# Kernel optimization log

Measured on AMD Instinct MI355X. Metric: run time of the kernel, lower is better.

The kernel has to match this reference:

```python
import jax, jax.numpy as jnp
import numpy as np

D_MODEL = 1024
NHEAD = 16
HEAD_DIM = D_MODEL // NHEAD


def setup_inputs() -> dict:
    key = jax.random.key(0)
    ks = jax.random.split(key, 11)
    B, T = 2, 2048
    s = 1.0 / np.sqrt(D_MODEL)
    return {
        "query": jax.random.normal(ks[0], (B, T, D_MODEL), jnp.float32),
        "key": jax.random.normal(ks[1], (B, T, D_MODEL), jnp.float32),
        "value": jax.random.normal(ks[2], (B, T, D_MODEL), jnp.float32),
        "Wq": jax.random.normal(ks[3], (D_MODEL, D_MODEL), jnp.float32) * s,
        "bq": jnp.zeros((D_MODEL,), jnp.float32),
        "Wk": jax.random.normal(ks[4], (D_MODEL, D_MODEL), jnp.float32) * s,
        "bk": jnp.zeros((D_MODEL,), jnp.float32),
        "Wv": jax.random.normal(ks[5], (D_MODEL, D_MODEL), jnp.float32) * s,
        "bv": jnp.zeros((D_MODEL,), jnp.float32),
        "Wo": jax.random.normal(ks[6], (D_MODEL, D_MODEL), jnp.float32) * s,
        "bo": jnp.zeros((D_MODEL,), jnp.float32),
    }


def reference(query, key, value, Wq, bq, Wk, bk, Wv, bv, Wo, bo):
    B, T, _ = query.shape
    scale = HEAD_DIM ** -0.5
    # Linear projections (torch Linear: x @ W.T + b)
    Q = query @ Wq.T + bq
    K = key @ Wk.T + bk
    V = value @ Wv.T + bv
    # [B, H, T, hd]
    Q = Q.reshape(B, T, NHEAD, HEAD_DIM).transpose(0, 2, 1, 3)
    K = K.reshape(B, T, NHEAD, HEAD_DIM).transpose(0, 2, 1, 3)
    V = V.reshape(B, T, NHEAD, HEAD_DIM).transpose(0, 2, 1, 3)
    # Attention scores [B, H, T, T]
    scores = jnp.einsum("bhqd,bhkd->bhqk", Q, K) * scale
    probs = jax.nn.softmax(scores, axis=-1)
    # dropout is identity in eval mode
    out = jnp.einsum("bhqk,bhkd->bhqd", probs, V)
    out = out.transpose(0, 2, 1, 3).reshape(B, T, D_MODEL)
    return out @ Wo.T + bo
```

## Files before the change

kernel.cpp:

```cpp
#include <hip/hip_runtime.h>
#include <stdint.h>

#define LOG2E_OVER_SQRTHD 0.18033688011112042f
#define SM_BIAS 12.0f

typedef unsigned short u16;
typedef _Float16 f16;
typedef __attribute__((ext_vector_type(4))) float f32x4;
typedef __attribute__((ext_vector_type(8))) _Float16 f16x8;

static __device__ __forceinline__ u16 f2h_bits(float f) {
  union { f16 h; u16 u; } v; v.h = (f16)f; return v.u;
}

static __device__ __forceinline__ void g2l16(const void* g, void* l) {
  __builtin_amdgcn_global_load_lds((const __attribute__((address_space(1))) void*)g,
                                   (__attribute__((address_space(3))) void*)l,
                                   16, 0, 0);
}

__global__ __launch_bounds__(256) void pack_all(
    const float* __restrict__ q, const float* __restrict__ k, const float* __restrict__ v,
    const float* __restrict__ wq, const float* __restrict__ wk,
    const float* __restrict__ wv, const float* __restrict__ wo,
    u16* __restrict__ X, u16* __restrict__ W) {
  int flat = blockIdx.x * 256 + threadIdx.x;
  const float* src;
  u16* dst;
  int idx;
  if (flat < 3 * 1048576) {
    int z = flat >> 20;
    idx = flat & 1048575;
    src = (z == 0) ? q : (z == 1) ? k : v;
    dst = X + (size_t)z * 4194304;
  } else {
    int f2 = flat - 3 * 1048576;
    int z = f2 >> 18;
    idx = f2 & 262143;
    src = (z == 0) ? wq : (z == 1) ? wk : (z == 2) ? wv : wo;
    dst = W + (size_t)z * 1048576;
  }
  float4 x = ((const float4*)src)[idx];
  ushort4 o;
  o.x = f2h_bits(x.x); o.y = f2h_bits(x.y); o.z = f2h_bits(x.z); o.w = f2h_bits(x.w);
  *(ushort4*)(dst + (size_t)idx * 4) = o;
}

template <bool OUT_F16>
static __device__ __forceinline__ void gemm_body(
    const u16* __restrict__ A, const u16* __restrict__ W,
    const float* __restrict__ bias, void* __restrict__ C,
    int ldc, bool row_bias, float oscale, int bm, int bn) {
  __shared__ u16 As[128 * 32];
  __shared__ u16 Bs[128 * 32];
  const int tid = threadIdx.x;
  const int lane = tid & 63;
  const int wave = tid >> 6;
  const int wm = wave >> 1, wn = wave & 1;
  const int quad = lane >> 4, l15 = lane & 15;

  f32x4 acc[4][4] = {};

  const int r0 = tid >> 2;
  const int c0 = (tid & 3) * 8;
  const u16* Ab = A + (size_t)bm * 1024;
  const u16* Wb = W + (size_t)bn * 1024;

  for (int kt = 0; kt < 32; ++kt) {
    const int kc = kt * 32;
    g2l16(Ab + (size_t)r0 * 1024 + kc + c0, As + tid * 8);
    g2l16(Ab + (size_t)(r0 + 64) * 1024 + kc + c0, As + (256 + tid) * 8);
    g2l16(Wb + (size_t)r0 * 1024 + kc + c0, Bs + tid * 8);
    g2l16(Wb + (size_t)(r0 + 64) * 1024 + kc + c0, Bs + (256 + tid) * 8);
    __syncthreads();
    f16x8 af[4], bw[4];
#pragma unroll
    for (int mt = 0; mt < 4; ++mt)
      af[mt] = *(const f16x8*)(As + (wm * 64 + mt * 16 + l15) * 32 + quad * 8);
#pragma unroll
    for (int nt = 0; nt < 4; ++nt)
      bw[nt] = *(const f16x8*)(Bs + (wn * 64 + nt * 16 + l15) * 32 + quad * 8);
#pragma unroll
    for (int mt = 0; mt < 4; ++mt)
#pragma unroll
      for (int nt = 0; nt < 4; ++nt)
        acc[mt][nt] = __builtin_amdgcn_mfma_f32_16x16x32_f16(af[mt], bw[nt], acc[mt][nt], 0, 0, 0);
    __syncthreads();
  }

#pragma unroll
  for (int mt = 0; mt < 4; ++mt) {
    const int row = bm + wm * 64 + mt * 16 + quad * 4;
#pragma unroll
    for (int nt = 0; nt < 4; ++nt) {
      const int col = bn + wn * 64 + nt * 16 + l15;
      const float bcol = row_bias ? 0.0f : bias[col];
#pragma unroll
      for (int i = 0; i < 4; ++i) {
        const float bb = row_bias ? bias[row + i] : bcol;
        float val = (acc[mt][nt][i] + bb) * oscale;
        if (OUT_F16)
          ((u16*)C)[(size_t)(row + i) * ldc + col] = f2h_bits(val);
        else
          ((float*)C)[(size_t)(row + i) * ldc + col] = val;
      }
    }
  }
}

__global__ __launch_bounds__(256) void gemm_qkv(const u16* __restrict__ X,
    const u16* __restrict__ Wf, const float* __restrict__ bq,
    const float* __restrict__ bk, const float* __restrict__ bv,
    u16* __restrict__ QK, u16* __restrict__ Vt, float qscale) {
  const int z = blockIdx.z;
  if (z == 0) {
    gemm_body<true>(X, Wf, bq, QK, 1024, false, qscale,
                    blockIdx.x * 128, blockIdx.y * 128);
  } else if (z == 1) {
    gemm_body<true>(X + (size_t)4194304, Wf + (size_t)1048576, bk,
                    QK + (size_t)4194304, 1024, false, 1.0f,
                    blockIdx.x * 128, blockIdx.y * 128);
  } else {
    gemm_body<true>(Wf + (size_t)2 * 1048576, X + (size_t)2 * 4194304, bv,
                    Vt, 4096, true, 1.0f,
                    blockIdx.y * 128, blockIdx.x * 128);
  }
}

__global__ __launch_bounds__(256) void gemm_out(const u16* __restrict__ O,
    const u16* __restrict__ Wo, const float* __restrict__ bo,
    float* __restrict__ out) {
  gemm_body<false>(O, Wo, bo, out, 1024, false, 1.0f,
                   blockIdx.x * 128, blockIdx.y * 128);
}

__global__ __launch_bounds__(256) void attn_kernel(const u16* __restrict__ QK,
                                                   const u16* __restrict__ Vt,
                                                   u16* __restrict__ O) {
  constexpr int LSP = 68;
  __shared__ u16 Qs[64 * 64];
  __shared__ u16 Ks[64 * 64];
  __shared__ u16 Vts[64 * 64];
  __shared__ u16 Ps[4][16 * LSP];

  const u16* Qb = QK;
  const u16* Kb = QK + (size_t)4096 * 1024;

  const int tid = threadIdx.x, lane = tid & 63, wave = tid >> 6;
  const int quad = lane >> 4, l15 = lane & 15;
  const int qt = blockIdx.x, h = blockIdx.y, b = blockIdx.z;
  const size_t qrow0 = (size_t)b * 2048 + qt * 64;
  const size_t kv0 = (size_t)b * 2048;
  const int hc = h * 64;

  const int r0 = tid >> 3;
  const int p0 = tid & 7;
  const int s0 = (p0 ^ (r0 & 7)) * 8;

  g2l16(Qb + (qrow0 + r0) * 1024 + hc + s0, Qs + tid * 8);
  g2l16(Qb + (qrow0 + 32 + r0) * 1024 + hc + s0, Qs + (256 + tid) * 8);
  __syncthreads();

  const int Rq = wave * 16 + l15;
  const f16x8 aq0 = *(const f16x8*)(Qs + Rq * 64 + ((quad ^ (Rq & 7)) * 8));
  const f16x8 aq1 = *(const f16x8*)(Qs + Rq * 64 + (((quad + 4) ^ (Rq & 7)) * 8));

  f32x4 o_acc[4] = {};
  float l_part[4] = {0.f, 0.f, 0.f, 0.f};
  u16* Pw = Ps[wave];

  for (int kt = 0; kt < 32; ++kt) {
    const size_t kr0 = kv0 + (size_t)kt * 64;
    __syncthreads();
    g2l16(Kb + (kr0 + r0) * 1024 + hc + s0, Ks + tid * 8);
    g2l16(Kb + (kr0 + 32 + r0) * 1024 + hc + s0, Ks + (256 + tid) * 8);
    g2l16(Vt + (size_t)(hc + r0) * 4096 + kr0 + s0, Vts + tid * 8);
    g2l16(Vt + (size_t)(hc + 32 + r0) * 4096 + kr0 + s0, Vts + (256 + tid) * 8);
    __syncthreads();

    f32x4 s[4];
#pragma unroll
    for (int nt = 0; nt < 4; ++nt)
      s[nt] = f32x4{-SM_BIAS, -SM_BIAS, -SM_BIAS, -SM_BIAS};
#pragma unroll
    for (int nt = 0; nt < 4; ++nt) {
      const int Rk = nt * 16 + l15;
      f16x8 bk0 = *(const f16x8*)(Ks + Rk * 64 + ((quad ^ (Rk & 7)) * 8));
      f16x8 bk1 = *(const f16x8*)(Ks + Rk * 64 + (((quad + 4) ^ (Rk & 7)) * 8));
      s[nt] = __builtin_amdgcn_mfma_f32_16x16x32_f16(aq0, bk0, s[nt], 0, 0, 0);
      s[nt] = __builtin_amdgcn_mfma_f32_16x16x32_f16(aq1, bk1, s[nt], 0, 0, 0);
    }

#pragma unroll
    for (int nt = 0; nt < 4; ++nt)
#pragma unroll
      for (int i = 0; i < 4; ++i) {
        float p = __builtin_amdgcn_exp2f(s[nt][i]);
        l_part[i] += p;
        Pw[(quad * 4 + i) * LSP + nt * 16 + l15] = f2h_bits(p);
      }
    asm volatile("s_waitcnt lgkmcnt(0)" ::: "memory");

    union { f16x8 v; struct { uint2 lo, hi; } h; } ap0, ap1;
    ap0.h.lo = *(const uint2*)(Pw + l15 * LSP + quad * 8);
    ap0.h.hi = *(const uint2*)(Pw + l15 * LSP + quad * 8 + 4);
    ap1.h.lo = *(const uint2*)(Pw + l15 * LSP + 32 + quad * 8);
    ap1.h.hi = *(const uint2*)(Pw + l15 * LSP + 32 + quad * 8 + 4);
#pragma unroll
    for (int ct = 0; ct < 4; ++ct) {
      const int Rv = ct * 16 + l15;
      f16x8 bv0 = *(const f16x8*)(Vts + Rv * 64 + ((quad ^ (Rv & 7)) * 8));
      f16x8 bv1 = *(const f16x8*)(Vts + Rv * 64 + (((quad + 4) ^ (Rv & 7)) * 8));
      o_acc[ct] = __builtin_amdgcn_mfma_f32_16x16x32_f16(ap0.v, bv0, o_acc[ct], 0, 0, 0);
      o_acc[ct] = __builtin_amdgcn_mfma_f32_16x16x32_f16(ap1.v, bv1, o_acc[ct], 0, 0, 0);
    }
  }

#pragma unroll
  for (int i = 0; i < 4; ++i)
#pragma unroll
    for (int d = 1; d < 16; d <<= 1) l_part[i] += __shfl_xor(l_part[i], d);

#pragma unroll
  for (int i = 0; i < 4; ++i) {
    const float inv = 1.0f / l_part[i];
    const size_t row = qrow0 + wave * 16 + quad * 4 + i;
#pragma unroll
    for (int ct = 0; ct < 4; ++ct) {
      float ov = o_acc[ct][i] * inv;
      int col = hc + ct * 16 + l15;
      O[row * 1024 + col] = f2h_bits(ov);
    }
  }
}

extern "C" void kernel_launch(void* const* d_in, const int* in_sizes, int n_in,
                              void* d_out, int out_size, void* d_ws, size_t ws_size,
                              hipStream_t stream) {
  const float* query = (const float*)d_in[0];
  const float* key   = (const float*)d_in[1];
  const float* value = (const float*)d_in[2];
  const float* Wq = (const float*)d_in[3];
  const float* bq = (const float*)d_in[4];
  const float* Wk = (const float*)d_in[5];
  const float* bk = (const float*)d_in[6];
  const float* Wv = (const float*)d_in[7];
  const float* bv = (const float*)d_in[8];
  const float* Wo = (const float*)d_in[9];
  const float* bo = (const float*)d_in[10];
  float* out = (float*)d_out;

  u16* X  = (u16*)d_ws;
  u16* W  = X + (size_t)3 * 4194304;
  u16* QK = W + (size_t)4 * 1048576;
  u16* Vt = QK + (size_t)2 * 4194304;
  u16* O  = X;

  pack_all<<<dim3(16384, 1, 1), 256, 0, stream>>>(query, key, value, Wq, Wk, Wv, Wo, X, W);
  gemm_qkv<<<dim3(32, 8, 3), 256, 0, stream>>>(X, W, bq, bk, bv, QK, Vt,
                                               LOG2E_OVER_SQRTHD);
  attn_kernel<<<dim3(32, 16, 2), 256, 0, stream>>>(QK, Vt, O);
  gemm_out<<<dim3(32, 8, 1), 256, 0, stream>>>(O, W + (size_t)3 * 1048576, bo, out);
}
```

Baseline: 253.3 us.

## Double-buffer LDS tiles in the projection GEMMs and the attention loop

The GEMM body and the attention kernel now keep two LDS buffers for the streamed operands (A/W tiles, and K/Vt tiles). The next K-step's global-to-LDS loads are issued before computing on the current buffer, with one barrier per iteration instead of two. The aim is to overlap global memory latency with MFMA work. In exchange, LDS use roughly doubles for these tiles, which may lower occupancy, especially in the attention kernel.

```diff
diff --git a/kernel.cpp b/kernel.cpp
--- a/kernel.cpp
+++ b/kernel.cpp
@@ -51,8 +51,8 @@
     const u16* __restrict__ A, const u16* __restrict__ W,
     const float* __restrict__ bias, void* __restrict__ C,
     int ldc, bool row_bias, float oscale, int bm, int bn) {
-  __shared__ u16 As[128 * 32];
-  __shared__ u16 Bs[128 * 32];
+  __shared__ u16 As[2][128 * 32];
+  __shared__ u16 Bs[2][128 * 32];
   const int tid = threadIdx.x;
   const int lane = tid & 63;
   const int wave = tid >> 6;
@@ -63,23 +63,31 @@
 
   const int r0 = tid >> 2;
   const int c0 = (tid & 3) * 8;
-  const u16* Ab = A + (size_t)bm * 1024;
-  const u16* Wb = W + (size_t)bn * 1024;
+  const u16* Ab = A + (size_t)bm * 1024 + (size_t)r0 * 1024 + c0;
+  const u16* Wb = W + (size_t)bn * 1024 + (size_t)r0 * 1024 + c0;
+
+  g2l16(Ab, As[0] + tid * 8);
+  g2l16(Ab + 64 * 1024, As[0] + (256 + tid) * 8);
+  g2l16(Wb, Bs[0] + tid * 8);
+  g2l16(Wb + 64 * 1024, Bs[0] + (256 + tid) * 8);
+  __syncthreads();
 
   for (int kt = 0; kt < 32; ++kt) {
-    const int kc = kt * 32;
-    g2l16(Ab + (size_t)r0 * 1024 + kc + c0, As + tid * 8);
-    g2l16(Ab + (size_t)(r0 + 64) * 1024 + kc + c0, As + (256 + tid) * 8);
-    g2l16(Wb + (size_t)r0 * 1024 + kc + c0, Bs + tid * 8);
-    g2l16(Wb + (size_t)(r0 + 64) * 1024 + kc + c0, Bs + (256 + tid) * 8);
-    __syncthreads();
+    const int p = kt & 1;
+    if (kt + 1 < 32) {
+      const int kc = (kt + 1) * 32;
+      g2l16(Ab + kc, As[p ^ 1] + tid * 8);
+      g2l16(Ab + 64 * 1024 + kc, As[p ^ 1] + (256 + tid) * 8);
+      g2l16(Wb + kc, Bs[p ^ 1] + tid * 8);
+      g2l16(Wb + 64 * 1024 + kc, Bs[p ^ 1] + (256 + tid) * 8);
+    }
     f16x8 af[4], bw[4];
 #pragma unroll
     for (int mt = 0; mt < 4; ++mt)
-      af[mt] = *(const f16x8*)(As + (wm * 64 + mt * 16 + l15) * 32 + quad * 8);
+      af[mt] = *(const f16x8*)(As[p] + (wm * 64 + mt * 16 + l15) * 32 + quad * 8);
 #pragma unroll
     for (int nt = 0; nt < 4; ++nt)
-      bw[nt] = *(const f16x8*)(Bs + (wn * 64 + nt * 16 + l15) * 32 + quad * 8);
+      bw[nt] = *(const f16x8*)(Bs[p] + (wn * 64 + nt * 16 + l15) * 32 + quad * 8);
 #pragma unroll
     for (int mt = 0; mt < 4; ++mt)
 #pragma unroll
@@ -139,8 +147,8 @@
                                                    u16* __restrict__ O) {
   constexpr int LSP = 68;
   __shared__ u16 Qs[64 * 64];
-  __shared__ u16 Ks[64 * 64];
-  __shared__ u16 Vts[64 * 64];
+  __shared__ u16 Ks[2][64 * 64];
+  __shared__ u16 Vts[2][64 * 64];
   __shared__ u16 Ps[4][16 * LSP];
 
   const u16* Qb = QK;
@@ -157,8 +165,15 @@
   const int p0 = tid & 7;
   const int s0 = (p0 ^ (r0 & 7)) * 8;
 
+  const u16* Kbase = Kb + (kv0 + r0) * 1024 + hc + s0;
+  const u16* Vbase = Vt + (size_t)(hc + r0) * 4096 + kv0 + s0;
+
   g2l16(Qb + (qrow0 + r0) * 1024 + hc + s0, Qs + tid * 8);
   g2l16(Qb + (qrow0 + 32 + r0) * 1024 + hc + s0, Qs + (256 + tid) * 8);
+  g2l16(Kbase, Ks[0] + tid * 8);
+  g2l16(Kbase + 32 * 1024, Ks[0] + (256 + tid) * 8);
+  g2l16(Vbase, Vts[0] + tid * 8);
+  g2l16(Vbase + (size_t)32 * 4096, Vts[0] + (256 + tid) * 8);
   __syncthreads();
 
   const int Rq = wave * 16 + l15;
@@ -170,13 +185,15 @@
   u16* Pw = Ps[wave];
 
   for (int kt = 0; kt < 32; ++kt) {
-    const size_t kr0 = kv0 + (size_t)kt * 64;
-    __syncthreads();
-    g2l16(Kb + (kr0 + r0) * 1024 + hc + s0, Ks + tid * 8);
-    g2l16(Kb + (kr0 + 32 + r0) * 1024 + hc + s0, Ks + (256 + tid) * 8);
-    g2l16(Vt + (size_t)(hc + r0) * 4096 + kr0 + s0, Vts + tid * 8);
-    g2l16(Vt + (size_t)(hc + 32 + r0) * 4096 + kr0 + s0, Vts + (256 + tid) * 8);
-    __syncthreads();
+    const int p = kt & 1;
+    if (kt + 1 < 32) {
+      const u16* Kn = Kbase + (size_t)(kt + 1) * 64 * 1024;
+      const u16* Vn = Vbase + (size_t)(kt + 1) * 64;
+      g2l16(Kn, Ks[p ^ 1] + tid * 8);
+      g2l16(Kn + 32 * 1024, Ks[p ^ 1] + (256 + tid) * 8);
+      g2l16(Vn, Vts[p ^ 1] + tid * 8);
+      g2l16(Vn + (size_t)32 * 4096, Vts[p ^ 1] + (256 + tid) * 8);
+    }
 
     f32x4 s[4];
 #pragma unroll
@@ -185,8 +202,8 @@
 #pragma unroll
     for (int nt = 0; nt < 4; ++nt) {
       const int Rk = nt * 16 + l15;
-      f16x8 bk0 = *(const f16x8*)(Ks + Rk * 64 + ((quad ^ (Rk & 7)) * 8));
-      f16x8 bk1 = *(const f16x8*)(Ks + Rk * 64 + (((quad + 4) ^ (Rk & 7)) * 8));
+      f16x8 bk0 = *(const f16x8*)(Ks[p] + Rk * 64 + ((quad ^ (Rk & 7)) * 8));
+      f16x8 bk1 = *(const f16x8*)(Ks[p] + Rk * 64 + (((quad + 4) ^ (Rk & 7)) * 8));
       s[nt] = __builtin_amdgcn_mfma_f32_16x16x32_f16(aq0, bk0, s[nt], 0, 0, 0);
       s[nt] = __builtin_amdgcn_mfma_f32_16x16x32_f16(aq1, bk1, s[nt], 0, 0, 0);
     }
@@ -195,9 +212,9 @@
     for (int nt = 0; nt < 4; ++nt)
 #pragma unroll
       for (int i = 0; i < 4; ++i) {
-        float p = __builtin_amdgcn_exp2f(s[nt][i]);
-        l_part[i] += p;
-        Pw[(quad * 4 + i) * LSP + nt * 16 + l15] = f2h_bits(p);
+        float pe = __builtin_amdgcn_exp2f(s[nt][i]);
+        l_part[i] += pe;
+        Pw[(quad * 4 + i) * LSP + nt * 16 + l15] = f2h_bits(pe);
       }
     asm volatile("s_waitcnt lgkmcnt(0)" ::: "memory");
 
@@ -209,11 +226,13 @@
 #pragma unroll
     for (int ct = 0; ct < 4; ++ct) {
       const int Rv = ct * 16 + l15;
-      f16x8 bv0 = *(const f16x8*)(Vts + Rv * 64 + ((quad ^ (Rv & 7)) * 8));
-      f16x8 bv1 = *(const f16x8*)(Vts + Rv * 64 + (((quad + 4) ^ (Rv & 7)) * 8));
+      f16x8 bv0 = *(const f16x8*)(Vts[p] + Rv * 64 + ((quad ^ (Rv & 7)) * 8));
+      f16x8 bv1 = *(const f16x8*)(Vts[p] + Rv * 64 + (((quad + 4) ^ (Rv & 7)) * 8));
       o_acc[ct] = __builtin_amdgcn_mfma_f32_16x16x32_f16(ap0.v, bv0, o_acc[ct], 0, 0, 0);
       o_acc[ct] = __builtin_amdgcn_mfma_f32_16x16x32_f16(ap1.v, bv1, o_acc[ct], 0, 0, 0);
     }
+
+    __syncthreads();
   }
 
 #pragma unroll
```

Result: slower. 265.4 us (+4.8%).
